# Kernel tuning notes

Measured on AMD Instinct MI355X. Metric: run time of the kernel, lower is better.

The kernel has to match this reference:

```python
import math
import jax, jax.numpy as jnp
import numpy as np

CAPACITY_FACTOR = 1.0
MIN_CAPACITY = 4


def setup_inputs() -> dict:
    key = jax.random.key(0)
    k1, k2 = jax.random.split(key)
    x = jax.random.normal(k1, (8192, 1024), dtype=jnp.float32)
    wg = jax.random.normal(k2, (1024, 64), dtype=jnp.float32) * 0.02
    return {"x": x, "wg": wg}


def reference(x, wg):
    # Gate projection: [S, D] @ [D, E] -> [S, E]
    logits = x @ wg
    S, E = logits.shape
    # _capacity: ceil(S / E * capacity_factor * 2) for top-2, floored at min_capacity (static)
    capacity = max(math.ceil((S / E) * (CAPACITY_FACTOR * 2.0)), MIN_CAPACITY)

    gates = jax.nn.softmax(logits, axis=-1)           # [S, E]
    org_gates = gates

    # top-1 expert
    indices1_s = jnp.argmax(gates, axis=1)
    mask1 = jax.nn.one_hot(indices1_s, E, dtype=jnp.int32)
    # top-2 expert (deterministic: no gumbel sampling)
    logits_except1 = jnp.where(mask1.astype(bool), -jnp.inf, logits)
    indices2_s = jnp.argmax(logits_except1, axis=1)
    mask2 = jax.nn.one_hot(indices2_s, E, dtype=jnp.int32)

    # per-expert running positions
    locations1 = jnp.cumsum(mask1, axis=0) - 1        # [S, E]
    locations2 = jnp.cumsum(mask2, axis=0) - 1 + jnp.sum(mask1, axis=0, keepdims=True)

    # load-balancing aux loss
    me = jnp.mean(gates, axis=0)
    ce = jnp.mean(mask1.astype(gates.dtype), axis=0)
    l_aux = jnp.sum(me * ce) * E * E

    exp_counts = jnp.sum(mask1 + mask2, axis=0)

    # drop tokens over capacity
    mask1 = mask1 * (locations1 < capacity).astype(jnp.int32)
    mask2 = mask2 * (locations2 < capacity).astype(jnp.int32)

    locations1_s = jnp.sum(locations1 * mask1, axis=1)  # [S]
    locations2_s = jnp.sum(locations2 * mask2, axis=1)

    mask1_f = mask1.astype(gates.dtype)
    mask2_f = mask2.astype(gates.dtype)
    gates1_s = jnp.sum(gates * mask1_f, axis=1)
    gates2_s = jnp.sum(gates * mask2_f, axis=1)
    denom_s = jnp.clip(gates1_s + gates2_s, jnp.finfo(gates.dtype).eps)
    gates1_s = gates1_s / denom_s
    gates2_s = gates2_s / denom_s

    gates1 = gates1_s[:, None] * mask1_f              # [S, E]
    gates2 = gates2_s[:, None] * mask2_f

    locations1_sc = jax.nn.one_hot(locations1_s, capacity, dtype=gates.dtype)  # [S, C]
    locations2_sc = jax.nn.one_hot(locations2_s, capacity, dtype=gates.dtype)

    combine_weights = (jnp.einsum('se,sc->sec', gates1, locations1_sc)
                       + jnp.einsum('se,sc->sec', gates2, locations2_sc))  # [S, E, C]
    dispatch_mask = combine_weights.astype(bool)
    return l_aux, combine_weights, dispatch_mask, exp_counts, org_gates
```

## Files before the change

kernel.cpp:

```cpp
#include <hip/hip_runtime.h>
#include <math.h>

#define S_TOKENS 8192
#define D_DIM    1024
#define E_EXP    64
#define CAPACITY 256
#define TPB      32
#define NBLK     (S_TOKENS / TPB)
#define NZBLK    4096

#define SZ_COMBINE   (134217728LL)
#define OFF_COMBINE  (1LL)
#define OFF_DISPATCH (OFF_COMBINE + SZ_COMBINE)
#define OFF_EXPCNT   (OFF_DISPATCH + SZ_COMBINE)
#define OFF_ORGGATES (OFF_EXPCNT + E_EXP)

#define WS_IDX1 0
#define WS_IDX2 (WS_IDX1 + S_TOKENS)
#define WS_G1   (WS_IDX2 + S_TOKENS)
#define WS_G2   (WS_G1 + S_TOKENS)
#define WS_CNT1 (WS_G2 + S_TOKENS)
#define WS_CNT2 (WS_CNT1 + NBLK * E_EXP)
#define WS_OFF1 (WS_CNT2 + NBLK * E_EXP)
#define WS_OFF2 (WS_OFF1 + NBLK * E_EXP)
#define WS_MEP  (WS_OFF2 + NBLK * E_EXP)

__global__ __launch_bounds__(256) void k1_gemm_gate(
    const float* __restrict__ x, const float* __restrict__ wg,
    float* __restrict__ out, int* __restrict__ wsi, float* __restrict__ wsf) {
  const int bid = blockIdx.x;
  const int tid = threadIdx.x;

  if (bid >= NBLK) {
    float4 z = make_float4(0.f, 0.f, 0.f, 0.f);
    float4* p = (float4*)out;
    const size_t n4 = (size_t)(2 * SZ_COMBINE) / 4;
    const size_t nth = (size_t)NZBLK * 256;
    for (size_t i = (size_t)(bid - NBLK) * 256 + tid; i < n4; i += nth) p[i] = z;
    if (bid == NBLK && tid == 0) out[2 * SZ_COMBINE] = 0.0f;
    return;
  }

  __shared__ float xs[TPB][64];
  __shared__ float wsh[64][64];
  __shared__ float Lg[TPB][65];
  __shared__ float mM[TPB], rS[TPB];
  __shared__ int   li1[TPB], li2[TPB];
  __shared__ float mered[4][64];

  const int e  = tid & 63;
  const int tg = tid >> 6;
  const int s0 = bid * TPB;

  float acc[8];
#pragma unroll
  for (int j = 0; j < 8; j++) acc[j] = 0.f;

  for (int k0 = 0; k0 < D_DIM; k0 += 64) {
    for (int i = tid; i < TPB * 16; i += 256) {
      int t = i >> 4, c = i & 15;
      ((float4*)&xs[t][0])[c] =
          *(const float4*)&x[(size_t)(s0 + t) * D_DIM + k0 + 4 * c];
    }
    for (int i = tid; i < 64 * 16; i += 256) {
      int kk = i >> 4, c = i & 15;
      ((float4*)&wsh[kk][0])[c] =
          *(const float4*)&wg[(size_t)(k0 + kk) * E_EXP + 4 * c];
    }
    __syncthreads();
#pragma unroll 8
    for (int kk = 0; kk < 64; kk++) {
      float w = wsh[kk][e];
#pragma unroll
      for (int j = 0; j < 8; j++)
        acc[j] = fmaf(xs[tg + 4 * j][kk], w, acc[j]);
    }
    __syncthreads();
  }

#pragma unroll
  for (int j = 0; j < 8; j++) Lg[tg + 4 * j][e] = acc[j];
  __syncthreads();

  {
    const int g = tid >> 3;
    const int u = tid & 7;
    float bv = -INFINITY; int bi = 0;
#pragma unroll
    for (int i = 0; i < 8; i++) {
      int ee = u + 8 * i;
      float v = Lg[g][ee];
      if (v > bv) { bv = v; bi = ee; }
    }
#pragma unroll
    for (int d = 1; d < 8; d <<= 1) {
      float ov = __shfl_xor(bv, d, 8);
      int   oi = __shfl_xor(bi, d, 8);
      if (ov > bv || (ov == bv && oi < bi)) { bv = ov; bi = oi; }
    }
    const float m1 = bv; const int i1 = bi;

    float se = 0.f;
#pragma unroll
    for (int i = 0; i < 8; i++) se += expf(Lg[g][u + 8 * i] - m1);
#pragma unroll
    for (int d = 1; d < 8; d <<= 1) se += __shfl_xor(se, d, 8);

    float bv2 = -INFINITY; int bi2 = 0;
#pragma unroll
    for (int i = 0; i < 8; i++) {
      int ee = u + 8 * i;
      float v = Lg[g][ee];
      if (ee != i1 && v > bv2) { bv2 = v; bi2 = ee; }
    }
#pragma unroll
    for (int d = 1; d < 8; d <<= 1) {
      float ov = __shfl_xor(bv2, d, 8);
      int   oi = __shfl_xor(bi2, d, 8);
      if (ov > bv2 || (ov == bv2 && oi < bi2)) { bv2 = ov; bi2 = oi; }
    }

    if (u == 0) {
      float rs = 1.0f / se;
      mM[g] = m1; rS[g] = rs;
      li1[g] = i1; li2[g] = bi2;
      int s = s0 + g;
      wsi[WS_IDX1 + s] = i1;
      wsi[WS_IDX2 + s] = bi2;
      wsf[WS_G1 + s] = rs;
      wsf[WS_G2 + s] = expf(bv2 - m1) * rs;
    }
  }
  __syncthreads();

  {
    float mes = 0.f;
#pragma unroll
    for (int j = 0; j < 8; j++) {
      int t = tg + 4 * j;
      float gate = expf(Lg[t][e] - mM[t]) * rS[t];
      out[OFF_ORGGATES + (size_t)(s0 + t) * E_EXP + e] = gate;
      mes += gate;
    }
    mered[tg][e] = mes;
  }
  __syncthreads();

  if (tid < 64) {
    wsf[WS_MEP + bid * 64 + tid] =
        mered[0][tid] + mered[1][tid] + mered[2][tid] + mered[3][tid];
    int c1 = 0, c2 = 0;
    for (int t = 0; t < TPB; t++) {
      c1 += (li1[t] == tid);
      c2 += (li2[t] == tid);
    }
    wsi[WS_CNT1 + bid * 64 + tid] = c1;
    wsi[WS_CNT2 + bid * 64 + tid] = c2;
  }
}

__global__ __launch_bounds__(1024) void k2_scan(
    float* __restrict__ out, int* __restrict__ wsi, float* __restrict__ wsf) {
  __shared__ int lc[NBLK * E_EXP];
  __shared__ float mep[16][E_EXP];
  __shared__ int tot1[E_EXP];

  const int tid = threadIdx.x;

  {
    const int e = tid & 63, cg = tid >> 6;
    float s = 0.f;
#pragma unroll
    for (int c = cg * 16; c < cg * 16 + 16; c++)
      s += wsf[WS_MEP + c * 64 + e];
    mep[cg][e] = s;
  }

  {
    const int4* g = (const int4*)&wsi[WS_CNT1];
    int4* l = (int4*)lc;
#pragma unroll
    for (int i = tid; i < NBLK * E_EXP / 4; i += 1024) l[i] = g[i];
  }
  __syncthreads();

  if (tid < E_EXP) {
    int run = 0;
#pragma unroll 8
    for (int c = 0; c < NBLK; c++) {
      wsi[WS_OFF1 + c * 64 + tid] = run;
      run += lc[c * 64 + tid];
    }
    tot1[tid] = run;
  }
  __syncthreads();

  {
    const int4* g = (const int4*)&wsi[WS_CNT2];
    int4* l = (int4*)lc;
#pragma unroll
    for (int i = tid; i < NBLK * E_EXP / 4; i += 1024) l[i] = g[i];
  }
  __syncthreads();

  if (tid < E_EXP) {
    const int e = tid;
    const int total1 = tot1[e];
    int run = total1;
#pragma unroll 8
    for (int c = 0; c < NBLK; c++) {
      wsi[WS_OFF2 + c * 64 + e] = run;
      run += lc[c * 64 + e];
    }
    const int total2 = run - total1;

    out[OFF_EXPCNT + e] = (float)(total1 + total2);

    float mesum = 0.f;
#pragma unroll
    for (int cg = 0; cg < 16; cg++) mesum += mep[cg][e];
    float me = mesum * (1.0f / 8192.0f);
    float ce = (float)total1 * (1.0f / 8192.0f);
    float prod = me * ce * 4096.0f;
#pragma unroll
    for (int d = 1; d < 64; d <<= 1) prod += __shfl_xor(prod, d, 64);
    if (e == 0) out[0] = prod;
  }
}

__global__ __launch_bounds__(64) void k3_scatter(
    float* __restrict__ out, const int* __restrict__ wsi,
    const float* __restrict__ wsf) {
  __shared__ int li1[TPB], li2[TPB];
  const int bid = blockIdx.x;
  const int t = threadIdx.x;
  const int s0 = bid * TPB;

  if (t < TPB) {
    li1[t] = wsi[WS_IDX1 + s0 + t];
    li2[t] = wsi[WS_IDX2 + s0 + t];
  }
  __syncthreads();
  if (t >= TPB) return;

  const int e1 = li1[t], e2 = li2[t];
  int r1 = 0, r2 = 0;
  for (int j = 0; j < t; j++) {
    r1 += (li1[j] == e1);
    r2 += (li2[j] == e2);
  }
  const int loc1 = wsi[WS_OFF1 + bid * 64 + e1] + r1;
  const int loc2 = wsi[WS_OFF2 + bid * 64 + e2] + r2;
  const int s = s0 + t;

  const float g1r = wsf[WS_G1 + s];
  const float g2r = wsf[WS_G2 + s];
  const bool d1 = (loc1 >= CAPACITY);
  const bool d2 = (loc2 >= CAPACITY);
  const float g1f = d1 ? 0.f : g1r;
  const float g2f = d2 ? 0.f : g2r;
  const float denom = fmaxf(g1f + g2f, 1.1920929e-7f);
  const float w1 = g1f / denom;
  const float w2 = g2f / denom;

  if (!d1) {
    size_t o = OFF_COMBINE + (size_t)s * (E_EXP * CAPACITY) +
               (size_t)e1 * CAPACITY + loc1;
    out[o] = w1;
    out[o + SZ_COMBINE] = (w1 != 0.f) ? 1.f : 0.f;
  }
  if (!d2) {
    size_t o = OFF_COMBINE + (size_t)s * (E_EXP * CAPACITY) +
               (size_t)e2 * CAPACITY + loc2;
    out[o] = w2;
    out[o + SZ_COMBINE] = (w2 != 0.f) ? 1.f : 0.f;
  }
}

extern "C" void kernel_launch(void* const* d_in, const int* in_sizes, int n_in,
                              void* d_out, int out_size, void* d_ws,
                              size_t ws_size, hipStream_t stream) {
  const float* x  = (const float*)d_in[0];
  const float* wg = (const float*)d_in[1];
  float* out = (float*)d_out;
  int*   wsi = (int*)d_ws;
  float* wsf = (float*)d_ws;

  hipLaunchKernelGGL(k1_gemm_gate, dim3(NBLK + NZBLK), dim3(256), 0, stream,
                     x, wg, out, wsi, wsf);
  hipLaunchKernelGGL(k2_scan, dim3(1), dim3(1024), 0, stream, out, wsi, wsf);
  hipLaunchKernelGGL(k3_scatter, dim3(NBLK), dim3(64), 0, stream, out, wsi,
                     wsf);
}
```

Before: 1.133 ms.

## Use 64-token register-tiled gate GEMM with nontemporal zero-fill stores

Doubles tokens per block to 64 and replaces the per-thread column GEMM with a 4x4 register tile using vector LDS loads, raising FMA-to-load ratio and halving redundant weight tile loads. Shared memory for weights and logits is overlapped, softmax/top-2 uses 4 lanes per token, and the scan and scatter kernels are adjusted for the new block count. The zero-fill of the large combine/dispatch output now uses nontemporal stores to avoid polluting cache. Fewer GEMM blocks may reduce parallelism, but the runtime is likely dominated by the 1 GB zero-fill anyway.

```diff
diff --git a/kernel.cpp b/kernel.cpp
--- a/kernel.cpp
+++ b/kernel.cpp
@@ -5,9 +5,11 @@
 #define D_DIM    1024
 #define E_EXP    64
 #define CAPACITY 256
-#define TPB      32
+#define TPB      64
 #define NBLK     (S_TOKENS / TPB)
 #define NZBLK    4096
+
+typedef float fx4 __attribute__((ext_vector_type(4)));
 
 #define SZ_COMBINE   (134217728LL)
 #define OFF_COMBINE  (1LL)
@@ -32,92 +34,110 @@
   const int tid = threadIdx.x;
 
   if (bid >= NBLK) {
-    float4 z = make_float4(0.f, 0.f, 0.f, 0.f);
-    float4* p = (float4*)out;
+    fx4 z = (fx4)0.f;
+    fx4* p = (fx4*)out;
     const size_t n4 = (size_t)(2 * SZ_COMBINE) / 4;
     const size_t nth = (size_t)NZBLK * 256;
-    for (size_t i = (size_t)(bid - NBLK) * 256 + tid; i < n4; i += nth) p[i] = z;
+    for (size_t i = (size_t)(bid - NBLK) * 256 + tid; i < n4; i += nth)
+      __builtin_nontemporal_store(z, &p[i]);
     if (bid == NBLK && tid == 0) out[2 * SZ_COMBINE] = 0.0f;
     return;
   }
 
-  __shared__ float xs[TPB][64];
-  __shared__ float wsh[64][64];
-  __shared__ float Lg[TPB][65];
-  __shared__ float mM[TPB], rS[TPB];
-  __shared__ int   li1[TPB], li2[TPB];
-  __shared__ float mered[4][64];
-
-  const int e  = tid & 63;
-  const int tg = tid >> 6;
+  __shared__ float xs[64][68];
+  __shared__ float ovl[64 * 68];
+  __shared__ float mM[64], rS[64];
+  __shared__ int   li1[64], li2[64];
+  __shared__ float mered[16][64];
+
+  float (*wsh)[64] = (float(*)[64])ovl;
+  float (*Lg)[68]  = (float(*)[68])ovl;
+
+  const int tx = tid & 15;
+  const int ty = tid >> 4;
   const int s0 = bid * TPB;
 
-  float acc[8];
-#pragma unroll
-  for (int j = 0; j < 8; j++) acc[j] = 0.f;
+  float acc[4][4];
+#pragma unroll
+  for (int i = 0; i < 4; i++)
+#pragma unroll
+    for (int q = 0; q < 4; q++) acc[i][q] = 0.f;
 
   for (int k0 = 0; k0 < D_DIM; k0 += 64) {
-    for (int i = tid; i < TPB * 16; i += 256) {
+#pragma unroll
+    for (int r = 0; r < 4; r++) {
+      int i = tid + 256 * r;
       int t = i >> 4, c = i & 15;
-      ((float4*)&xs[t][0])[c] =
-          *(const float4*)&x[(size_t)(s0 + t) * D_DIM + k0 + 4 * c];
-    }
-    for (int i = tid; i < 64 * 16; i += 256) {
-      int kk = i >> 4, c = i & 15;
-      ((float4*)&wsh[kk][0])[c] =
-          *(const float4*)&wg[(size_t)(k0 + kk) * E_EXP + 4 * c];
+      *(fx4*)&xs[t][4 * c] =
+          *(const fx4*)&x[(size_t)(s0 + t) * D_DIM + k0 + 4 * c];
+      *(fx4*)&wsh[t][4 * c] =
+          *(const fx4*)&wg[(size_t)(k0 + t) * E_EXP + 4 * c];
     }
     __syncthreads();
-#pragma unroll 8
-    for (int kk = 0; kk < 64; kk++) {
-      float w = wsh[kk][e];
-#pragma unroll
-      for (int j = 0; j < 8; j++)
-        acc[j] = fmaf(xs[tg + 4 * j][kk], w, acc[j]);
+    for (int kb = 0; kb < 64; kb += 4) {
+      fx4 xa[4], wb[4];
+#pragma unroll
+      for (int i = 0; i < 4; i++) xa[i] = *(fx4*)&xs[ty + 16 * i][kb];
+#pragma unroll
+      for (int j = 0; j < 4; j++) wb[j] = *(fx4*)&wsh[kb + j][4 * tx];
+#pragma unroll
+      for (int j = 0; j < 4; j++)
+#pragma unroll
+        for (int i = 0; i < 4; i++) {
+          float xv = xa[i][j];
+#pragma unroll
+          for (int q = 0; q < 4; q++)
+            acc[i][q] = fmaf(xv, wb[j][q], acc[i][q]);
+        }
     }
     __syncthreads();
   }
 
 #pragma unroll
-  for (int j = 0; j < 8; j++) Lg[tg + 4 * j][e] = acc[j];
-  __syncthreads();
-
-  {
-    const int g = tid >> 3;
-    const int u = tid & 7;
+  for (int i = 0; i < 4; i++) {
+    fx4 v;
+#pragma unroll
+    for (int q = 0; q < 4; q++) v[q] = acc[i][q];
+    *(fx4*)&Lg[ty + 16 * i][4 * tx] = v;
+  }
+  __syncthreads();
+
+  {
+    const int g = tid >> 2;
+    const int u = tid & 3;
     float bv = -INFINITY; int bi = 0;
 #pragma unroll
-    for (int i = 0; i < 8; i++) {
-      int ee = u + 8 * i;
+    for (int i = 0; i < 16; i++) {
+      int ee = u + 4 * i;
       float v = Lg[g][ee];
       if (v > bv) { bv = v; bi = ee; }
     }
 #pragma unroll
-    for (int d = 1; d < 8; d <<= 1) {
-      float ov = __shfl_xor(bv, d, 8);
-      int   oi = __shfl_xor(bi, d, 8);
-      if (ov > bv || (ov == bv && oi < bi)) { bv = ov; bi = oi; }
+    for (int d = 1; d < 4; d <<= 1) {
+      float ovv = __shfl_xor(bv, d, 4);
+      int   oi  = __shfl_xor(bi, d, 4);
+      if (ovv > bv || (ovv == bv && oi < bi)) { bv = ovv; bi = oi; }
     }
     const float m1 = bv; const int i1 = bi;
 
     float se = 0.f;
 #pragma unroll
-    for (int i = 0; i < 8; i++) se += expf(Lg[g][u + 8 * i] - m1);
-#pragma unroll
-    for (int d = 1; d < 8; d <<= 1) se += __shfl_xor(se, d, 8);
+    for (int i = 0; i < 16; i++) se += expf(Lg[g][u + 4 * i] - m1);
+#pragma unroll
+    for (int d = 1; d < 4; d <<= 1) se += __shfl_xor(se, d, 4);
 
     float bv2 = -INFINITY; int bi2 = 0;
 #pragma unroll
-    for (int i = 0; i < 8; i++) {
-      int ee = u + 8 * i;
+    for (int i = 0; i < 16; i++) {
+      int ee = u + 4 * i;
       float v = Lg[g][ee];
       if (ee != i1 && v > bv2) { bv2 = v; bi2 = ee; }
     }
 #pragma unroll
-    for (int d = 1; d < 8; d <<= 1) {
-      float ov = __shfl_xor(bv2, d, 8);
-      int   oi = __shfl_xor(bi2, d, 8);
-      if (ov > bv2 || (ov == bv2 && oi < bi2)) { bv2 = ov; bi2 = oi; }
+    for (int d = 1; d < 4; d <<= 1) {
+      float ovv = __shfl_xor(bv2, d, 4);
+      int   oi  = __shfl_xor(bi2, d, 4);
+      if (ovv > bv2 || (ovv == bv2 && oi < bi2)) { bv2 = ovv; bi2 = oi; }
     }
 
     if (u == 0) {
@@ -134,21 +154,29 @@
   __syncthreads();
 
   {
-    float mes = 0.f;
-#pragma unroll
-    for (int j = 0; j < 8; j++) {
-      int t = tg + 4 * j;
-      float gate = expf(Lg[t][e] - mM[t]) * rS[t];
-      out[OFF_ORGGATES + (size_t)(s0 + t) * E_EXP + e] = gate;
-      mes += gate;
-    }
-    mered[tg][e] = mes;
+    float ms[4] = {0.f, 0.f, 0.f, 0.f};
+#pragma unroll
+    for (int i = 0; i < 4; i++) {
+      int t = ty + 16 * i;
+      float m = mM[t], r = rS[t];
+      size_t ob = OFF_ORGGATES + (size_t)(s0 + t) * E_EXP + 4 * tx;
+#pragma unroll
+      for (int q = 0; q < 4; q++) {
+        float gate = expf(Lg[t][4 * tx + q] - m) * r;
+        out[ob + q] = gate;
+        ms[q] += gate;
+      }
+    }
+#pragma unroll
+    for (int q = 0; q < 4; q++) mered[ty][4 * tx + q] = ms[q];
   }
   __syncthreads();
 
   if (tid < 64) {
-    wsf[WS_MEP + bid * 64 + tid] =
-        mered[0][tid] + mered[1][tid] + mered[2][tid] + mered[3][tid];
+    float s = 0.f;
+#pragma unroll
+    for (int yy = 0; yy < 16; yy++) s += mered[yy][tid];
+    wsf[WS_MEP + bid * 64 + tid] = s;
     int c1 = 0, c2 = 0;
     for (int t = 0; t < TPB; t++) {
       c1 += (li1[t] == tid);
@@ -171,8 +199,7 @@
     const int e = tid & 63, cg = tid >> 6;
     float s = 0.f;
 #pragma unroll
-    for (int c = cg * 16; c < cg * 16 + 16; c++)
-      s += wsf[WS_MEP + c * 64 + e];
+    for (int c = cg * 8; c < cg * 8 + 8; c++) s += wsf[WS_MEP + c * 64 + e];
     mep[cg][e] = s;
   }
 
@@ -236,12 +263,9 @@
   const int t = threadIdx.x;
   const int s0 = bid * TPB;
 
-  if (t < TPB) {
-    li1[t] = wsi[WS_IDX1 + s0 + t];
-    li2[t] = wsi[WS_IDX2 + s0 + t];
-  }
-  __syncthreads();
-  if (t >= TPB) return;
+  li1[t] = wsi[WS_IDX1 + s0 + t];
+  li2[t] = wsi[WS_IDX2 + s0 + t];
+  __syncthreads();
 
   const int e1 = li1[t], e2 = li2[t];
   int r1 = 0, r2 = 0;
```

Measured after the change: 1.134 ms (median of 2 runs). No clear change (+0.1%).
